# Kernel tuning notes

Hardware: AMD Instinct MI355X
Metric: run time of the kernel (lower is better)

## Reference

```python
import math
import jax, jax.numpy as jnp
import numpy as np

B, S, D = 4, 2048, 1024
NEG = -1e20

def setup_inputs() -> dict:
    key = jax.random.key(0)
    k1, k2, k3, k4 = jax.random.split(key, 4)
    X = jax.random.normal(k1, (B, S, D), dtype=jnp.float32)
    # True = masked position (masked_fill semantics)
    attention_mask = jax.random.randint(k2, (B, S, S), 0, 2).astype(bool)
    scale = 1.0 / math.sqrt(D)
    W_qkv = jax.random.normal(k3, (D, 3 * D), dtype=jnp.float32) * scale
    b_qkv = jnp.zeros((3 * D,), dtype=jnp.float32)
    W_out = jax.random.normal(k4, (D, D), dtype=jnp.float32) * scale
    b_out = jnp.zeros((D,), dtype=jnp.float32)
    return {"X": X, "attention_mask": attention_mask,
            "W_qkv": W_qkv, "b_qkv": b_qkv, "W_out": W_out, "b_out": b_out}

def reference(X, attention_mask, W_qkv, b_qkv, W_out, b_out):
    dim = X.shape[-1]
    QKV = X @ W_qkv + b_qkv                      # [B,S,3D]
    Q, K, V = jnp.split(QKV, 3, axis=-1)         # each [B,S,D]
    scores = jnp.einsum('bqd,bkd->bqk', Q, K) / math.sqrt(dim)  # [B,S,S]
    scores = jnp.where(attention_mask, NEG, scores)
    attn = jax.nn.softmax(scores, axis=-1)       # dropout_rate=0.0 -> identity
    ctx = jnp.einsum('bqk,bkd->bqd', attn, V)    # [B,S,D]
    return ctx @ W_out + b_out
```

## Files before the change

### kernel.cpp

```cpp
#include <hip/hip_runtime.h>
#include <cstdint>
#include <cstddef>

#define BB 4
#define SS 2048
#define DD 1024

typedef _Float16 f16;
typedef _Float16 f16x8 __attribute__((ext_vector_type(8)));
typedef _Float16 f16x4 __attribute__((ext_vector_type(4)));
typedef float fx4 __attribute__((ext_vector_type(4)));

__device__ __forceinline__ void async_copy16(void* lds, const void* g) {
  __builtin_amdgcn_global_load_lds(
      (__attribute__((address_space(1))) void*)const_cast<void*>(g),
      (__attribute__((address_space(3))) void*)lds,
      16, 0, 0);
}

enum { EPI_BIAS = 0, EPI_MASKEXP = 1, EPI_ROWSCALE = 2, EPI_QKV = 3 };

template <typename OutT, int MODE>
__global__ __launch_bounds__(512, 2) void gemm_nt8(
    const f16* __restrict__ A, long long strideA, int lda,
    const f16* __restrict__ Bt, long long strideB, int ldb,
    OutT* __restrict__ C, long long strideC, int ldc,
    const float* __restrict__ bias, const uint32_t* __restrict__ gmask,
    float* __restrict__ rowSum, f16* __restrict__ vt, float scale, int K) {
  __shared__ __align__(16) char smem[131072];

  const int t = threadIdx.x;
  const int lane = t & 63;
  const int wid = t >> 6;
  const long long bz = blockIdx.z;
  const int tileM = blockIdx.y * 256;
  const int tileN = blockIdx.x * 256;

  const f16* Ab = A + bz * strideA;
  const f16* Bb = Bt + bz * strideB;
  OutT* Cb = C + bz * strideC;

  const int gch = ((t & 3) ^ ((t >> 3) & 3)) * 8;
  const f16* pA = Ab + (size_t)(tileM + (t >> 2)) * lda + gch;
  const f16* pB = Bb + (size_t)(tileN + (t >> 2)) * ldb + gch;
  const size_t rA = (size_t)128 * lda;
  const size_t rB = (size_t)128 * ldb;
  const int tb = t * 16;

  const int waveM = (wid >> 2) * 128;
  const int waveN = (wid & 3) * 64;
  const int r16 = lane & 15;
  const int quad = lane >> 4;
  const int sw = (r16 >> 1) & 3;

  const int nT = K >> 6;

#define STG_A(par, ks, Tn)                                      \
  {                                                             \
    char* d_ = smem + (par) * 65536 + (ks) * 16384;             \
    const f16* s_ = pA + (size_t)(Tn) * 64 + (ks) * 32;         \
    async_copy16(d_ + tb, s_);                                  \
    async_copy16(d_ + 8192 + tb, s_ + rA);                      \
  }
#define STG_B(par, ks, Tn)                                      \
  {                                                             \
    char* d_ = smem + (par) * 65536 + 32768 + (ks) * 16384;     \
    const f16* s_ = pB + (size_t)(Tn) * 64 + (ks) * 32;         \
    async_copy16(d_ + tb, s_);                                  \
    async_copy16(d_ + 8192 + tb, s_ + rB);                      \
  }

  STG_A(0, 0, 0);
  STG_B(0, 0, 0);
  STG_A(0, 1, 0);
  STG_B(0, 1, 0);
  asm volatile("s_waitcnt vmcnt(4)" ::: "memory");
  __builtin_amdgcn_s_barrier();
  __builtin_amdgcn_sched_barrier(0);

  fx4 acc[8][4] = {};
  f16x8 af[4], bf[4];

#define LOADB(Bs)                                                              \
  _Pragma("unroll") for (int j = 0; j < 4; ++j) bf[j] =                        \
      *(const f16x8*)&(Bs)[(waveN + j * 16 + r16) * 32 + (quad ^ sw) * 8];
#define LOADA(As, mo)                                                          \
  _Pragma("unroll") for (int m = 0; m < 4; ++m) af[m] =                        \
      *(const f16x8*)&(As)[(waveM + (mo) + m * 16 + r16) * 32 + (quad ^ sw) * 8];
#define MFMA16(mo)                                                             \
  __builtin_amdgcn_s_setprio(1);                                               \
  _Pragma("unroll") for (int m = 0; m < 4; ++m)                                \
  _Pragma("unroll") for (int j = 0; j < 4; ++j)                                \
      acc[(mo) + m][j] = __builtin_amdgcn_mfma_f32_16x16x32_f16(               \
          af[m], bf[j], acc[(mo) + m][j], 0, 0, 0);                            \
  __builtin_amdgcn_s_setprio(0);

  for (int T = 0; T < nT; ++T) {
    const int par = T & 1;
    const int np = par ^ 1;
    const bool st = (T + 1) < nT;
    const f16* As0 = (const f16*)(smem + par * 65536);
    const f16* As1 = As0 + 8192;
    const f16* Bs0 = As0 + 16384;
    const f16* Bs1 = As0 + 24576;

    LOADB(Bs0);
    LOADA(As0, 0);
    if (st) STG_A(np, 0, T + 1);
    __builtin_amdgcn_s_barrier();
    MFMA16(0);
    __builtin_amdgcn_s_barrier();

    LOADA(As0, 64);
    if (st) STG_B(np, 0, T + 1);
    __builtin_amdgcn_s_barrier();
    MFMA16(4);
    if (st) {
      asm volatile("s_waitcnt vmcnt(4)" ::: "memory");
    } else {
      asm volatile("s_waitcnt vmcnt(0)" ::: "memory");
    }
    __builtin_amdgcn_s_barrier();
    __builtin_amdgcn_sched_barrier(0);

    LOADB(Bs1);
    LOADA(As1, 0);
    if (st) STG_A(np, 1, T + 1);
    __builtin_amdgcn_s_barrier();
    MFMA16(0);
    __builtin_amdgcn_s_barrier();

    LOADA(As1, 64);
    if (st) STG_B(np, 1, T + 1);
    __builtin_amdgcn_s_barrier();
    MFMA16(4);
    if (st) {
      asm volatile("s_waitcnt vmcnt(4)" ::: "memory");
    }
    __builtin_amdgcn_s_barrier();
    __builtin_amdgcn_sched_barrier(0);
  }

  if constexpr (MODE == EPI_BIAS) {
#pragma unroll
    for (int j = 0; j < 4; ++j) {
      const int col = tileN + waveN + j * 16 + r16;
      const float bv = bias[col];
#pragma unroll
      for (int m = 0; m < 8; ++m) {
#pragma unroll
        for (int r = 0; r < 4; ++r) {
          const int row = tileM + waveM + m * 16 + quad * 4 + r;
          Cb[(size_t)row * ldc + col] = (OutT)(acc[m][j][r] * scale + bv);
        }
      }
    }
  } else if constexpr (MODE == EPI_QKV) {
    if (tileN < 2 * DD) {
#pragma unroll
      for (int j = 0; j < 4; ++j) {
        const int col = tileN + waveN + j * 16 + r16;
        const float bv = bias[col];
#pragma unroll
        for (int m = 0; m < 8; ++m) {
#pragma unroll
          for (int r = 0; r < 4; ++r) {
            const int row = tileM + waveM + m * 16 + quad * 4 + r;
            Cb[(size_t)row * ldc + col] = (OutT)(acc[m][j][r] + bv);
          }
        }
      }
    } else {
      const int b = tileM >> 11;
      const int s0 = (tileM & 2047) + waveM;
      f16* vb = vt + (size_t)b * DD * SS;
#pragma unroll
      for (int j = 0; j < 4; ++j) {
        const int col = tileN + waveN + j * 16 + r16;
        const float bv = bias[col];
        const int d = col - 2 * DD;
#pragma unroll
        for (int m = 0; m < 8; ++m) {
          const int s = s0 + m * 16 + quad * 4;
          f16x4 v4;
#pragma unroll
          for (int r = 0; r < 4; ++r) v4[r] = (f16)(acc[m][j][r] + bv);
          *(f16x4*)&vb[(size_t)d * SS + s] = v4;
        }
      }
    }
  } else if constexpr (MODE == EPI_MASKEXP) {
#pragma unroll
    for (int m = 0; m < 8; ++m) {
#pragma unroll
      for (int r = 0; r < 4; ++r) {
        const int row = tileM + waveM + m * 16 + quad * 4 + r;
        const uint32_t* gr =
            gmask + (((size_t)bz * SS + row) << 6) + ((tileN + waveN) >> 5);
        const uint32_t w0 = gr[0], w1 = gr[1];
        float part = 0.0f;
#pragma unroll
        for (int j = 0; j < 4; ++j) {
          const int bitpos = j * 16 + r16;
          const uint32_t mv = ((j < 2 ? w0 : w1) >> (bitpos & 31)) & 1u;
          const float e = mv ? 0.0f : __expf(acc[m][j][r] * scale);
          Cb[(size_t)row * ldc + tileN + waveN + j * 16 + r16] = (OutT)e;
          part += e;
        }
#pragma unroll
        for (int d = 1; d < 16; d <<= 1) part += __shfl_xor(part, d, 64);
        if (r16 == 0) atomicAdd(&rowSum[bz * SS + row], part);
      }
    }
  } else {
#pragma unroll
    for (int m = 0; m < 8; ++m) {
#pragma unroll
      for (int r = 0; r < 4; ++r) {
        const int row = tileM + waveM + m * 16 + quad * 4 + r;
        const float inv = scale / rowSum[bz * SS + row];
#pragma unroll
        for (int j = 0; j < 4; ++j) {
          const int col = tileN + waveN + j * 16 + r16;
          Cb[(size_t)row * ldc + col] = (OutT)(acc[m][j][r] * inv);
        }
      }
    }
  }
#undef STG_A
#undef STG_B
#undef LOADB
#undef LOADA
#undef MFMA16
}

__global__ __launch_bounds__(256) void k_prep(
    const float* __restrict__ X, f16* __restrict__ Xh,
    const float* __restrict__ Wqkv, f16* __restrict__ Wqkvt,
    const float* __restrict__ Wout, f16* __restrict__ Woutt,
    float* __restrict__ rowSum, const int* __restrict__ mask,
    uint32_t* __restrict__ gmask) {
  int bid = blockIdx.x;
  const int t = threadIdx.x;
  if (bid < 8192) {
    const int i = bid * 256 + t;
    const float4 v = ((const float4*)X)[i];
    f16x4 h = {(f16)v.x, (f16)v.y, (f16)v.z, (f16)v.w};
    ((f16x4*)Xh)[i] = h;
    return;
  }
  bid -= 8192;
  __shared__ float tile[32][33];
  const int tx = t & 31, ty = t >> 5;
  if (bid < 3072) {
    const int bx = (bid % 96) * 32, by = (bid / 96) * 32;
    for (int i2 = ty; i2 < 32; i2 += 8)
      tile[i2][tx] = Wqkv[(size_t)(by + i2) * 3072 + bx + tx];
    __syncthreads();
    for (int i2 = ty; i2 < 32; i2 += 8)
      Wqkvt[(size_t)(bx + i2) * 1024 + by + tx] = (f16)tile[tx][i2];
    return;
  }
  bid -= 3072;
  if (bid < 1024) {
    const int bx = (bid & 31) * 32, by = (bid >> 5) * 32;
    for (int i2 = ty; i2 < 32; i2 += 8)
      tile[i2][tx] = Wout[(size_t)(by + i2) * 1024 + bx + tx];
    __syncthreads();
    for (int i2 = ty; i2 < 32; i2 += 8)
      Woutt[(size_t)(bx + i2) * 1024 + by + tx] = (f16)tile[tx][i2];
    return;
  }
  bid -= 1024;
  if (bid < 32) {
    rowSum[bid * 256 + t] = 0.0f;
    return;
  }
  bid -= 32;
  const int w = bid * 256 + t;
  const int4* mr = (const int4*)(mask + ((size_t)w << 5));
  uint32_t v = 0;
#pragma unroll
  for (int c = 0; c < 8; ++c) {
    const int4 q = mr[c];
    v |= (q.x ? 1u : 0u) << (c * 4);
    v |= (q.y ? 1u : 0u) << (c * 4 + 1);
    v |= (q.z ? 1u : 0u) << (c * 4 + 2);
    v |= (q.w ? 1u : 0u) << (c * 4 + 3);
  }
  gmask[w] = v;
}

extern "C" void kernel_launch(void* const* d_in, const int* in_sizes, int n_in,
                              void* d_out, int out_size, void* d_ws, size_t ws_size,
                              hipStream_t stream) {
  const float* X = (const float*)d_in[0];
  const int* mask = (const int*)d_in[1];
  const float* Wqkv = (const float*)d_in[2];
  const float* bqkv = (const float*)d_in[3];
  const float* Wout = (const float*)d_in[4];
  const float* bout = (const float*)d_in[5];
  float* out = (float*)d_out;

  char* ws = (char*)d_ws;
  f16* Xh = (f16*)(ws + 0);
  f16* Wqkvt = (f16*)(ws + 16777216);
  f16* Woutt = (f16*)(ws + 23068672);
  f16* QK = (f16*)(ws + 25165824);
  f16* Vt = (f16*)(ws + 58720256);
  f16* E = (f16*)(ws + 75497472);
  f16* Ctx = (f16*)(ws + 109051904);
  float* rowSum = (float*)(ws + 125829120);
  uint32_t* gmask = (uint32_t*)(ws + 109051904);

  k_prep<<<dim3(14368), dim3(256), 0, stream>>>(X, Xh, Wqkv, Wqkvt, Wout, Woutt,
                                                rowSum, mask, gmask);

  gemm_nt8<f16, EPI_QKV><<<dim3(12, 32, 1), dim3(512), 0, stream>>>(
      Xh, 0LL, DD, Wqkvt, 0LL, DD, QK, 0LL, 2 * DD, bqkv, nullptr, nullptr, Vt,
      1.0f, DD);

  gemm_nt8<f16, EPI_MASKEXP><<<dim3(8, 8, 4), dim3(512), 0, stream>>>(
      QK, (long long)SS * 2 * DD, 2 * DD, QK + DD, (long long)SS * 2 * DD, 2 * DD,
      E, (long long)SS * SS, SS, nullptr, gmask, rowSum, nullptr, 0.03125f, DD);

  gemm_nt8<f16, EPI_ROWSCALE><<<dim3(4, 8, 4), dim3(512), 0, stream>>>(
      E, (long long)SS * SS, SS, Vt, (long long)DD * SS, SS, Ctx,
      (long long)SS * DD, DD, nullptr, nullptr, rowSum, nullptr, 1.0f, SS);

  gemm_nt8<float, EPI_BIAS><<<dim3(4, 32, 1), dim3(512), 0, stream>>>(
      Ctx, 0LL, DD, Woutt, 0LL, DD, out, 0LL, DD, bout, nullptr, nullptr, nullptr,
      1.0f, DD);
}
```

Before: 372.4 us.

## Use 128x128-tile GEMM for PV and output projections; pin schedule in 256-tile kernel

Adds a smaller gemm_nt kernel with 256 threads, 128x128 tiles and a simple double-buffered K loop. The attention-times-V GEMM and the output projection now use it, giving 512 blocks each instead of 128 so the GPU's many CUs have more to work on. The large 256-tile kernel gains explicit sched_barriers and lgkmcnt(0) waits around its barriers to pin instruction order, and its unused epilogues are dropped. Smaller tiles mean less data reuse and more global and LDS traffic per FLOP. The extra waits may also serialize LDS reads with MFMA work.

```diff
diff --git a/kernel.cpp b/kernel.cpp
--- a/kernel.cpp
+++ b/kernel.cpp
@@ -19,6 +19,113 @@
 }
 
 enum { EPI_BIAS = 0, EPI_MASKEXP = 1, EPI_ROWSCALE = 2, EPI_QKV = 3 };
+
+template <typename OutT, int MODE>
+__global__ __launch_bounds__(256, 2) void gemm_nt(
+    const f16* __restrict__ A, long long strideA, int lda,
+    const f16* __restrict__ Bt, long long strideB, int ldb,
+    OutT* __restrict__ C, long long strideC, int ldc,
+    const float* __restrict__ bias, const int* __restrict__ mask,
+    float* __restrict__ rowSum, f16* __restrict__ vt, float scale, int K) {
+  constexpr int SMEM_BYTES = 32768;
+  __shared__ __align__(16) char smem[SMEM_BYTES];
+
+  const int t = threadIdx.x;
+  const int lane = t & 63;
+  const int wid = t >> 6;
+  const long long bz = blockIdx.z;
+  const int tileM = blockIdx.y * 128;
+  const int tileN = blockIdx.x * 128;
+
+  const f16* Ab = A + bz * strideA;
+  const f16* Bb = Bt + bz * strideB;
+  OutT* Cb = C + bz * strideC;
+
+  const int sr = t >> 2;
+  const int sc = (((t & 3) ^ ((t >> 3) & 3)) * 8);
+  const f16* pa0 = Ab + (size_t)(tileM + sr) * lda + sc;
+  const f16* pa1 = Ab + (size_t)(tileM + 64 + sr) * lda + sc;
+  const f16* pb0 = Bb + (size_t)(tileN + sr) * ldb + sc;
+  const f16* pb1 = Bb + (size_t)(tileN + 64 + sr) * ldb + sc;
+  const int tb = t * 16;
+
+  const int waveM = (wid >> 1) * 64;
+  const int waveN = (wid & 1) * 64;
+  const int r16 = lane & 15;
+  const int quad = lane >> 4;
+  const int sw = (r16 >> 1) & 3;
+
+  const int nIter = K >> 5;
+  {
+    char* b0 = smem;
+    async_copy16(b0 + tb, pa0);
+    async_copy16(b0 + 4096 + tb, pa1);
+    async_copy16(b0 + 8192 + tb, pb0);
+    async_copy16(b0 + 12288 + tb, pb1);
+  }
+
+  fx4 acc[4][4] = {};
+
+#pragma unroll 2
+  for (int i = 0; i < nIter; ++i) {
+    __syncthreads();
+    if (i + 1 < nIter) {
+      char* nb = smem + ((i + 1) & 1) * 16384;
+      const int k = (i + 1) << 5;
+      async_copy16(nb + tb, pa0 + k);
+      async_copy16(nb + 4096 + tb, pa1 + k);
+      async_copy16(nb + 8192 + tb, pb0 + k);
+      async_copy16(nb + 12288 + tb, pb1 + k);
+    }
+    const f16* As = (const f16*)(smem + (i & 1) * 16384);
+    const f16* Bs = As + 4096;
+
+    f16x8 af[4], bf[4];
+#pragma unroll
+    for (int x = 0; x < 4; ++x)
+      af[x] = *(const f16x8*)&As[(waveM + x * 16 + r16) * 32 + (quad ^ sw) * 8];
+#pragma unroll
+    for (int x = 0; x < 4; ++x)
+      bf[x] = *(const f16x8*)&Bs[(waveN + x * 16 + r16) * 32 + (quad ^ sw) * 8];
+
+#pragma unroll
+    for (int x = 0; x < 4; ++x)
+#pragma unroll
+      for (int j = 0; j < 4; ++j)
+        acc[x][j] =
+            __builtin_amdgcn_mfma_f32_16x16x32_f16(af[x], bf[j], acc[x][j], 0, 0, 0);
+  }
+
+  if constexpr (MODE == EPI_BIAS) {
+#pragma unroll
+    for (int j = 0; j < 4; ++j) {
+      const int col = tileN + waveN + j * 16 + r16;
+      const float bv = bias[col];
+#pragma unroll
+      for (int i = 0; i < 4; ++i) {
+#pragma unroll
+        for (int r = 0; r < 4; ++r) {
+          const int row = tileM + waveM + i * 16 + quad * 4 + r;
+          Cb[(size_t)row * ldc + col] = (OutT)(acc[i][j][r] * scale + bv);
+        }
+      }
+    }
+  } else {
+#pragma unroll
+    for (int i = 0; i < 4; ++i) {
+#pragma unroll
+      for (int r = 0; r < 4; ++r) {
+        const int row = tileM + waveM + i * 16 + quad * 4 + r;
+        const float inv = scale / rowSum[bz * SS + row];
+#pragma unroll
+        for (int j = 0; j < 4; ++j) {
+          const int col = tileN + waveN + j * 16 + r16;
+          Cb[(size_t)row * ldc + col] = (OutT)(acc[i][j][r] * inv);
+        }
+      }
+    }
+  }
+}
 
 template <typename OutT, int MODE>
 __global__ __launch_bounds__(512, 2) void gemm_nt8(
@@ -70,13 +177,16 @@
     async_copy16(d_ + 8192 + tb, s_ + rB);                      \
   }
 
+#define PIN() __builtin_amdgcn_sched_barrier(0)
+#define LGKM0() asm volatile("s_waitcnt lgkmcnt(0)" ::: "memory")
+
   STG_A(0, 0, 0);
   STG_B(0, 0, 0);
   STG_A(0, 1, 0);
   STG_B(0, 1, 0);
   asm volatile("s_waitcnt vmcnt(4)" ::: "memory");
   __builtin_amdgcn_s_barrier();
-  __builtin_amdgcn_sched_barrier(0);
+  PIN();
 
   fx4 acc[8][4] = {};
   f16x8 af[4], bf[4];
@@ -107,55 +217,59 @@
     LOADB(Bs0);
     LOADA(As0, 0);
     if (st) STG_A(np, 0, T + 1);
-    __builtin_amdgcn_s_barrier();
+    PIN();
+    __builtin_amdgcn_s_barrier();
+    LGKM0();
+    PIN();
     MFMA16(0);
-    __builtin_amdgcn_s_barrier();
+    PIN();
+    __builtin_amdgcn_s_barrier();
+    PIN();
 
     LOADA(As0, 64);
     if (st) STG_B(np, 0, T + 1);
-    __builtin_amdgcn_s_barrier();
+    PIN();
+    __builtin_amdgcn_s_barrier();
+    LGKM0();
+    PIN();
     MFMA16(4);
+    PIN();
     if (st) {
       asm volatile("s_waitcnt vmcnt(4)" ::: "memory");
     } else {
       asm volatile("s_waitcnt vmcnt(0)" ::: "memory");
     }
     __builtin_amdgcn_s_barrier();
-    __builtin_amdgcn_sched_barrier(0);
+    PIN();
 
     LOADB(Bs1);
     LOADA(As1, 0);
     if (st) STG_A(np, 1, T + 1);
-    __builtin_amdgcn_s_barrier();
+    PIN();
+    __builtin_amdgcn_s_barrier();
+    LGKM0();
+    PIN();
     MFMA16(0);
-    __builtin_amdgcn_s_barrier();
+    PIN();
+    __builtin_amdgcn_s_barrier();
+    PIN();
 
     LOADA(As1, 64);
     if (st) STG_B(np, 1, T + 1);
-    __builtin_amdgcn_s_barrier();
+    PIN();
+    __builtin_amdgcn_s_barrier();
+    LGKM0();
+    PIN();
     MFMA16(4);
+    PIN();
     if (st) {
       asm volatile("s_waitcnt vmcnt(4)" ::: "memory");
     }
     __builtin_amdgcn_s_barrier();
-    __builtin_amdgcn_sched_barrier(0);
-  }
-
-  if constexpr (MODE == EPI_BIAS) {
-#pragma unroll
-    for (int j = 0; j < 4; ++j) {
-      const int col = tileN + waveN + j * 16 + r16;
-      const float bv = bias[col];
-#pragma unroll
-      for (int m = 0; m < 8; ++m) {
-#pragma unroll
-        for (int r = 0; r < 4; ++r) {
-          const int row = tileM + waveM + m * 16 + quad * 4 + r;
-          Cb[(size_t)row * ldc + col] = (OutT)(acc[m][j][r] * scale + bv);
-        }
-      }
-    }
-  } else if constexpr (MODE == EPI_QKV) {
+    PIN();
+  }
+
+  if constexpr (MODE == EPI_QKV) {
     if (tileN < 2 * DD) {
 #pragma unroll
       for (int j = 0; j < 4; ++j) {
@@ -212,26 +326,14 @@
         if (r16 == 0) atomicAdd(&rowSum[bz * SS + row], part);
       }
     }
-  } else {
-#pragma unroll
-    for (int m = 0; m < 8; ++m) {
-#pragma unroll
-      for (int r = 0; r < 4; ++r) {
-        const int row = tileM + waveM + m * 16 + quad * 4 + r;
-        const float inv = scale / rowSum[bz * SS + row];
-#pragma unroll
-        for (int j = 0; j < 4; ++j) {
-          const int col = tileN + waveN + j * 16 + r16;
-          Cb[(size_t)row * ldc + col] = (OutT)(acc[m][j][r] * inv);
-        }
-      }
-    }
   }
 #undef STG_A
 #undef STG_B
 #undef LOADB
 #undef LOADA
 #undef MFMA16
+#undef PIN
+#undef LGKM0
 }
 
 __global__ __launch_bounds__(256) void k_prep(
@@ -324,11 +426,11 @@
       QK, (long long)SS * 2 * DD, 2 * DD, QK + DD, (long long)SS * 2 * DD, 2 * DD,
       E, (long long)SS * SS, SS, nullptr, gmask, rowSum, nullptr, 0.03125f, DD);
 
-  gemm_nt8<f16, EPI_ROWSCALE><<<dim3(4, 8, 4), dim3(512), 0, stream>>>(
+  gemm_nt<f16, EPI_ROWSCALE><<<dim3(8, 16, 4), dim3(256), 0, stream>>>(
       E, (long long)SS * SS, SS, Vt, (long long)DD * SS, SS, Ctx,
       (long long)SS * DD, DD, nullptr, nullptr, rowSum, nullptr, 1.0f, SS);
 
-  gemm_nt8<float, EPI_BIAS><<<dim3(4, 32, 1), dim3(512), 0, stream>>>(
+  gemm_nt<float, EPI_BIAS><<<dim3(8, 64, 1), dim3(256), 0, stream>>>(
       Ctx, 0LL, DD, Woutt, 0LL, DD, out, 0LL, DD, bout, nullptr, nullptr, nullptr,
       1.0f, DD);
 }
```

Measured after the change: 353.5 us. 1.05x faster.
